# Kernel optimization log

Hardware: AMD Instinct MI355X
Metric: run time of the kernel (lower is better)

## Reference

```python
import jax, jax.numpy as jnp
import numpy as np

FEATURES = 1024
HEAD_DIM = 64
NUM_HEADS = 16
EPS = 1e-5


def setup_inputs() -> dict:
    key = jax.random.key(0)
    ks = jax.random.split(key, 6)
    x = jax.random.normal(ks[0], (2, 2048, FEATURES), dtype=jnp.float32)
    s_in = 1.0 / np.sqrt(FEATURES)
    s_hd = 1.0 / np.sqrt(NUM_HEADS * HEAD_DIM)
    return {
        "x": x,
        "gamma": jnp.ones((FEATURES,), jnp.float32),
        "beta": jnp.zeros((FEATURES,), jnp.float32),
        "Wq": jax.random.normal(ks[1], (FEATURES, NUM_HEADS * HEAD_DIM), jnp.float32) * s_in,
        "Wkv": jax.random.normal(ks[2], (FEATURES, 2 * HEAD_DIM), jnp.float32) * s_in,
        "Wo": jax.random.normal(ks[3], (NUM_HEADS * HEAD_DIM, FEATURES), jnp.float32) * s_hd,
        "bo": jax.random.normal(ks[4], (FEATURES,), jnp.float32) * s_hd,
    }


def reference(x, gamma, beta, Wq, Wkv, Wo, bo):
    # LayerNorm over last dim
    mu = jnp.mean(x, axis=-1, keepdims=True)
    var = jnp.mean(jnp.square(x - mu), axis=-1, keepdims=True)
    xn = (x - mu) * jax.lax.rsqrt(var + EPS) * gamma + beta

    b, t, _ = x.shape
    q = (xn @ Wq).reshape(b, t, NUM_HEADS, HEAD_DIM).transpose(0, 2, 1, 3)  # b h t d
    kv = xn @ Wkv  # b s 2d
    k, v = kv[..., :HEAD_DIM], kv[..., HEAD_DIM:]  # b s d (single shared head)

    scale = HEAD_DIM ** (-0.5)
    attn = jnp.einsum('bhtd,bsd->bhts', q, k) * scale
    attn = jax.nn.softmax(attn, axis=-1)
    out = jnp.einsum('bhts,bsd->bhtd', attn, v)
    out = out.transpose(0, 2, 1, 3).reshape(b, t, NUM_HEADS * HEAD_DIM)
    return out @ Wo + bo + x
```

## Files before the change

### kernel.cpp

```cpp
#include <hip/hip_runtime.h>

typedef __attribute__((ext_vector_type(8))) __bf16 bf16x8;
typedef __attribute__((ext_vector_type(4))) float floatx4;
typedef unsigned short u16;
typedef unsigned int u32;

#define KSCALE 0.18033688011112042f

__device__ __forceinline__ u16 f2bf(float f) {
    union { float f; u32 u; } v; v.f = f;
    u32 r = v.u + 0x7fffu + ((v.u >> 16) & 1u);
    return (u16)(r >> 16);
}

__device__ __forceinline__ u32 pk2bf(float a, float b) {
    union { float f; u32 u; } x, y; x.f = a; y.f = b;
    return __builtin_amdgcn_perm(y.u + 0x8000u, x.u + 0x8000u, 0x07060302);
}

__device__ __forceinline__ void gl_lds16(const u16* g, u16* l) {
    __builtin_amdgcn_global_load_lds((const __attribute__((address_space(1))) void*)g,
                                     (__attribute__((address_space(3))) void*)l, 16, 0, 0);
}

__global__ __launch_bounds__(256) void prep(const float* __restrict__ Wq, const float* __restrict__ Wkv,
                                            const float* __restrict__ Wo, const float* __restrict__ x,
                                            const float* __restrict__ gamma, const float* __restrict__ beta,
                                            u16* __restrict__ WqkvT, u16* __restrict__ WoT,
                                            u16* __restrict__ xn) {
    __shared__ float tile[64][68];
    __shared__ float ps[4], ps2[4];
    const int bx = blockIdx.x;
    const int t = threadIdx.x;
    if (bx < 768) {
        const int z = bx >> 8, rem = bx & 255;
        const int tr = (rem >> 4) * 64, tc = (rem & 15) * 64;
        const float* in = (z == 0) ? Wq : (z == 1 ? Wkv : Wo);
        u16* out = (z == 0) ? WqkvT : (z == 1 ? WqkvT + (size_t)1024 * 1024 : WoT);
        const int cols = (z == 1) ? 128 : 1024;
        if (tc >= cols) return;
        for (int p = 0; p < 4; p++) {
            int ri = (t >> 4) + p * 16;
            int ci = (t & 15) * 4;
            float4 v = *(const float4*)&in[(size_t)(tr + ri) * cols + tc + ci];
            tile[ri][ci + 0] = v.x; tile[ri][ci + 1] = v.y;
            tile[ri][ci + 2] = v.z; tile[ri][ci + 3] = v.w;
        }
        __syncthreads();
        for (int p = 0; p < 4; p++) {
            int oc = (t >> 4) + p * 16;
            int ir = (t & 15) * 4;
            float s = (z == 1 && (tc + oc) < 64) ? KSCALE : 1.0f;
            ushort4 o;
            o.x = f2bf(tile[ir + 0][oc] * s);
            o.y = f2bf(tile[ir + 1][oc] * s);
            o.z = f2bf(tile[ir + 2][oc] * s);
            o.w = f2bf(tile[ir + 3][oc] * s);
            *(ushort4*)&out[(size_t)(tc + oc) * 1024 + tr + ir] = o;
        }
    } else {
        const int row = bx - 768;
        const float* xr = x + (size_t)row * 1024;
        float4 v = *(const float4*)&xr[t * 4];
        float s = v.x + v.y + v.z + v.w;
        float s2 = v.x * v.x + v.y * v.y + v.z * v.z + v.w * v.w;
        for (int off = 1; off < 64; off <<= 1) {
            s += __shfl_xor(s, off, 64);
            s2 += __shfl_xor(s2, off, 64);
        }
        int w = t >> 6, lane = t & 63;
        if (lane == 0) { ps[w] = s; ps2[w] = s2; }
        __syncthreads();
        float S = ps[0] + ps[1] + ps[2] + ps[3];
        float S2 = ps2[0] + ps2[1] + ps2[2] + ps2[3];
        float mu = S * (1.0f / 1024.0f);
        float var = S2 * (1.0f / 1024.0f) - mu * mu;
        float rstd = rsqrtf(var + 1e-5f);
        ushort4 o;
        o.x = f2bf((v.x - mu) * rstd * gamma[t * 4 + 0] + beta[t * 4 + 0]);
        o.y = f2bf((v.y - mu) * rstd * gamma[t * 4 + 1] + beta[t * 4 + 1]);
        o.z = f2bf((v.z - mu) * rstd * gamma[t * 4 + 2] + beta[t * 4 + 2]);
        o.w = f2bf((v.w - mu) * rstd * gamma[t * 4 + 3] + beta[t * 4 + 3]);
        *(ushort4*)&xn[(size_t)row * 1024 + t * 4] = o;
    }
}

template <bool FINAL>
__global__ __launch_bounds__(256) void gemm_bt(const u16* __restrict__ A, const u16* __restrict__ BT,
                                               u16* __restrict__ Cb, float* __restrict__ Cf,
                                               const float* __restrict__ bias, const float* __restrict__ resid,
                                               u16* __restrict__ vt2, int M, int N, int K) {
    __shared__ u16 as_[128 * 32];
    __shared__ u16 bs_[128 * 32];
    const int t = threadIdx.x;
    const int w = t >> 6, lane = t & 63, q = lane >> 4, c = lane & 15;
    const int tm = blockIdx.y * 128, tn = blockIdx.x * 128;
    const int wm = (w & 1) * 64, wn = (w >> 1) * 64;

    const int srow = lane >> 2, sch = (lane & 3) * 8;
    const u16* ag0 = A + (size_t)(tm + w * 16 + srow) * K + sch;
    const u16* ag1 = ag0 + (size_t)64 * K;
    const u16* bg0 = BT + (size_t)(tn + w * 16 + srow) * K + sch;
    const u16* bg1 = bg0 + (size_t)64 * K;
    u16* al0 = as_ + (w * 16) * 32;
    u16* al1 = as_ + (64 + w * 16) * 32;
    u16* bl0 = bs_ + (w * 16) * 32;
    u16* bl1 = bs_ + (64 + w * 16) * 32;

    floatx4 acc[4][4];
    for (int i = 0; i < 4; i++)
        for (int j = 0; j < 4; j++) acc[i][j] = (floatx4){0.f, 0.f, 0.f, 0.f};

    for (int k0 = 0; k0 < K; k0 += 32) {
        __syncthreads();
        gl_lds16(ag0 + k0, al0);
        gl_lds16(ag1 + k0, al1);
        gl_lds16(bg0 + k0, bl0);
        gl_lds16(bg1 + k0, bl1);
        __syncthreads();
        bf16x8 af[4], bf[4];
#pragma unroll
        for (int i = 0; i < 4; i++) af[i] = *(const bf16x8*)&as_[(wm + i * 16 + c) * 32 + q * 8];
#pragma unroll
        for (int j = 0; j < 4; j++) bf[j] = *(const bf16x8*)&bs_[(wn + j * 16 + c) * 32 + q * 8];
#pragma unroll
        for (int i = 0; i < 4; i++)
#pragma unroll
            for (int j = 0; j < 4; j++)
                acc[i][j] = __builtin_amdgcn_mfma_f32_16x16x32_bf16(af[i], bf[j], acc[i][j], 0, 0, 0);
    }
#pragma unroll
    for (int i = 0; i < 4; i++)
#pragma unroll
        for (int j = 0; j < 4; j++)
#pragma unroll
            for (int r = 0; r < 4; r++) {
                int row = tm + wm + i * 16 + q * 4 + r;
                int col = tn + wn + j * 16 + c;
                float v = acc[i][j][r];
                if (FINAL) {
                    Cf[(size_t)row * N + col] = v + bias[col] + resid[(size_t)row * N + col];
                } else if (col < 1088) {
                    Cb[(size_t)row * N + col] = f2bf(v);
                } else {
                    int d = col - 1088;
                    int bb = row >> 11, sl = row & 2047;
                    int Bk = sl >> 5, u = sl & 31;
                    int up = ((u >> 2) & 3) * 8 + ((u >> 4) << 2) + (u & 3);
                    vt2[((size_t)(bb * 64 + d)) * 2048 + Bk * 32 + up] = f2bf(v);
                }
            }
}

union Vf { bf16x8 v; u32 w[4]; };

__global__ __launch_bounds__(512, 4) void attn5(const u16* __restrict__ qkv, const u16* __restrict__ vt2,
                                                u16* __restrict__ out) {
    __shared__ u16 ksm[2][64 * 64];
    __shared__ u16 vsm[2][64 * 64];
    const int t = threadIdx.x;
    const int w = t >> 6, lane = t & 63;
    const int q = lane >> 4, c = lane & 15;
    const int qt = blockIdx.x, hg = blockIdx.y, b = blockIdx.z;
    const int h = hg * 8 + w;
    const size_t qrow0 = (size_t)b * 2048 + qt * 16;
    const u16* kbase = qkv + (size_t)b * 2048 * 1152 + 1024;
    const u16* vbase = vt2 + (size_t)b * 64 * 2048;

    const int srow = w * 8 + (lane >> 3);
    const int sch = lane & 7;
    const int swz = (sch ^ (srow & 7)) * 8;
    const u16* kg = kbase + (size_t)srow * 1152 + swz;
    const u16* vg = vbase + (size_t)srow * 2048 + swz;
    u16* kl[2] = {&ksm[0][(w * 8) * 64], &ksm[1][(w * 8) * 64]};
    u16* vl[2] = {&vsm[0][(w * 8) * 64], &vsm[1][(w * 8) * 64]};

    bf16x8 qf[2];
#pragma unroll
    for (int kk = 0; kk < 2; kk++)
        qf[kk] = *(const bf16x8*)&qkv[(qrow0 + c) * 1152 + h * 64 + kk * 32 + q * 8];

    floatx4 O[4], Lacc;
#pragma unroll
    for (int di = 0; di < 4; di++) O[di] = (floatx4){0.f, 0.f, 0.f, 0.f};
    Lacc = (floatx4){0.f, 0.f, 0.f, 0.f};
    Vf ones;
    ones.w[0] = ones.w[1] = ones.w[2] = ones.w[3] = 0x3F803F80u;

    gl_lds16(kg, kl[0]);
    gl_lds16(vg, vl[0]);
    __syncthreads();

    const int c7 = c & 7;
    for (int tt = 0; tt < 32; tt++) {
        const int cur = tt & 1, nxt = cur ^ 1;
        if (tt < 31) {
            gl_lds16(kg + (size_t)(tt + 1) * 64 * 1152, kl[nxt]);
            gl_lds16(vg + (tt + 1) * 64, vl[nxt]);
        }

        bf16x8 kf[4][2];
        Vf vf[4][2];
#pragma unroll
        for (int ni = 0; ni < 4; ni++)
#pragma unroll
            for (int kk = 0; kk < 2; kk++)
                kf[ni][kk] = *(const bf16x8*)&ksm[cur][(ni * 16 + c) * 64 + (((kk * 4 + q) ^ c7) * 8)];
#pragma unroll
        for (int di = 0; di < 4; di++)
#pragma unroll
            for (int kk = 0; kk < 2; kk++)
                vf[di][kk].v = *(const bf16x8*)&vsm[cur][(di * 16 + c) * 64 + (((kk * 4 + q) ^ c7) * 8)];

        floatx4 sacc[4];
#pragma unroll
        for (int ni = 0; ni < 4; ni++) {
            floatx4 z = (floatx4){0.f, 0.f, 0.f, 0.f};
            z = __builtin_amdgcn_mfma_f32_16x16x32_bf16(kf[ni][0], qf[0], z, 0, 0, 0);
            z = __builtin_amdgcn_mfma_f32_16x16x32_bf16(kf[ni][1], qf[1], z, 0, 0, 0);
            sacc[ni] = z;
        }

        u32 pk[4][2];
#pragma unroll
        for (int ni = 0; ni < 4; ni++) {
            float p0 = exp2f(sacc[ni][0]);
            float p1 = exp2f(sacc[ni][1]);
            float p2 = exp2f(sacc[ni][2]);
            float p3 = exp2f(sacc[ni][3]);
            pk[ni][0] = pk2bf(p0, p1);
            pk[ni][1] = pk2bf(p2, p3);
        }

#pragma unroll
        for (int kk = 0; kk < 2; kk++) {
            Vf pf;
            pf.w[0] = pk[2 * kk][0];
            pf.w[1] = pk[2 * kk][1];
            pf.w[2] = pk[2 * kk + 1][0];
            pf.w[3] = pk[2 * kk + 1][1];
#pragma unroll
            for (int di = 0; di < 4; di++)
                O[di] = __builtin_amdgcn_mfma_f32_16x16x32_bf16(vf[di][kk].v, pf.v, O[di], 0, 0, 0);
            Lacc = __builtin_amdgcn_mfma_f32_16x16x32_bf16(ones.v, pf.v, Lacc, 0, 0, 0);
        }

        __syncthreads();
    }

    float inv = 1.0f / Lacc[0];
#pragma unroll
    for (int di = 0; di < 4; di++) {
        ushort4 o;
        o.x = f2bf(O[di][0] * inv);
        o.y = f2bf(O[di][1] * inv);
        o.z = f2bf(O[di][2] * inv);
        o.w = f2bf(O[di][3] * inv);
        *(ushort4*)&out[(qrow0 + c) * 1024 + h * 64 + di * 16 + q * 4] = o;
    }
}

extern "C" void kernel_launch(void* const* d_in, const int* in_sizes, int n_in,
                              void* d_out, int out_size, void* d_ws, size_t ws_size,
                              hipStream_t stream) {
    const float* x = (const float*)d_in[0];
    const float* gamma = (const float*)d_in[1];
    const float* beta = (const float*)d_in[2];
    const float* Wq = (const float*)d_in[3];
    const float* Wkv = (const float*)d_in[4];
    const float* Wo = (const float*)d_in[5];
    const float* bo = (const float*)d_in[6];
    float* out = (float*)d_out;

    u16* WqkvT = (u16*)d_ws;
    u16* WoT = WqkvT + (size_t)1152 * 1024;
    u16* xn = WoT + (size_t)1024 * 1024;
    u16* qkv = xn + (size_t)4096 * 1024;
    u16* vt2 = qkv + (size_t)4096 * 1152;
    u16* attnO = xn;

    prep<<<4864, 256, 0, stream>>>(Wq, Wkv, Wo, x, gamma, beta, WqkvT, WoT, xn);
    gemm_bt<false><<<dim3(9, 32), 256, 0, stream>>>(xn, WqkvT, qkv, nullptr, nullptr, nullptr, vt2,
                                                    4096, 1152, 1024);
    attn5<<<dim3(128, 2, 2), 512, 0, stream>>>(qkv, vt2, attnO);
    gemm_bt<true><<<dim3(8, 32), 256, 0, stream>>>(attnO, WoT, nullptr, out, bo, x, nullptr,
                                                   4096, 1024, 1024);
}
```

Before: 199.9 us.

## Shrink GEMM M-tile to 64 and double attention KV chunk per barrier

The GEMM tile drops from 128x128 to 64x128 rows, which doubles the grid (288→576 and 256→512 blocks) so the machine's many CUs are better filled, at the cost of less operand reuse per block. The attention kernel now stages 128 keys and values per double-buffered step and processes them in two 64-key sub-steps, halving the number of barriers and load rounds. This doubles the attention LDS use to 64KB per block, which may reduce how many blocks fit per CU.

After: 187.5 us. -6.2%, faster.

```diff
diff --git a/kernel.cpp b/kernel.cpp
--- a/kernel.cpp
+++ b/kernel.cpp
@@ -90,47 +90,44 @@
                                                u16* __restrict__ Cb, float* __restrict__ Cf,
                                                const float* __restrict__ bias, const float* __restrict__ resid,
                                                u16* __restrict__ vt2, int M, int N, int K) {
-    __shared__ u16 as_[128 * 32];
+    __shared__ u16 as_[64 * 32];
     __shared__ u16 bs_[128 * 32];
     const int t = threadIdx.x;
     const int w = t >> 6, lane = t & 63, q = lane >> 4, c = lane & 15;
-    const int tm = blockIdx.y * 128, tn = blockIdx.x * 128;
-    const int wm = (w & 1) * 64, wn = (w >> 1) * 64;
+    const int tm = blockIdx.y * 64, tn = blockIdx.x * 128;
+    const int wm = (w & 1) * 32, wn = (w >> 1) * 64;
 
     const int srow = lane >> 2, sch = (lane & 3) * 8;
-    const u16* ag0 = A + (size_t)(tm + w * 16 + srow) * K + sch;
-    const u16* ag1 = ag0 + (size_t)64 * K;
+    const u16* ag = A + (size_t)(tm + w * 16 + srow) * K + sch;
     const u16* bg0 = BT + (size_t)(tn + w * 16 + srow) * K + sch;
     const u16* bg1 = bg0 + (size_t)64 * K;
-    u16* al0 = as_ + (w * 16) * 32;
-    u16* al1 = as_ + (64 + w * 16) * 32;
+    u16* al = as_ + (w * 16) * 32;
     u16* bl0 = bs_ + (w * 16) * 32;
     u16* bl1 = bs_ + (64 + w * 16) * 32;
 
-    floatx4 acc[4][4];
-    for (int i = 0; i < 4; i++)
+    floatx4 acc[2][4];
+    for (int i = 0; i < 2; i++)
         for (int j = 0; j < 4; j++) acc[i][j] = (floatx4){0.f, 0.f, 0.f, 0.f};
 
     for (int k0 = 0; k0 < K; k0 += 32) {
         __syncthreads();
-        gl_lds16(ag0 + k0, al0);
-        gl_lds16(ag1 + k0, al1);
+        gl_lds16(ag + k0, al);
         gl_lds16(bg0 + k0, bl0);
         gl_lds16(bg1 + k0, bl1);
         __syncthreads();
-        bf16x8 af[4], bf[4];
-#pragma unroll
-        for (int i = 0; i < 4; i++) af[i] = *(const bf16x8*)&as_[(wm + i * 16 + c) * 32 + q * 8];
+        bf16x8 af[2], bf[4];
+#pragma unroll
+        for (int i = 0; i < 2; i++) af[i] = *(const bf16x8*)&as_[(wm + i * 16 + c) * 32 + q * 8];
 #pragma unroll
         for (int j = 0; j < 4; j++) bf[j] = *(const bf16x8*)&bs_[(wn + j * 16 + c) * 32 + q * 8];
 #pragma unroll
-        for (int i = 0; i < 4; i++)
+        for (int i = 0; i < 2; i++)
 #pragma unroll
             for (int j = 0; j < 4; j++)
                 acc[i][j] = __builtin_amdgcn_mfma_f32_16x16x32_bf16(af[i], bf[j], acc[i][j], 0, 0, 0);
     }
 #pragma unroll
-    for (int i = 0; i < 4; i++)
+    for (int i = 0; i < 2; i++)
 #pragma unroll
         for (int j = 0; j < 4; j++)
 #pragma unroll
@@ -154,10 +151,10 @@
 
 union Vf { bf16x8 v; u32 w[4]; };
 
-__global__ __launch_bounds__(512, 4) void attn5(const u16* __restrict__ qkv, const u16* __restrict__ vt2,
+__global__ __launch_bounds__(512, 4) void attn6(const u16* __restrict__ qkv, const u16* __restrict__ vt2,
                                                 u16* __restrict__ out) {
-    __shared__ u16 ksm[2][64 * 64];
-    __shared__ u16 vsm[2][64 * 64];
+    __shared__ u16 ksm[2][128 * 64];
+    __shared__ u16 vsm[2][2 * 64 * 64];
     const int t = threadIdx.x;
     const int w = t >> 6, lane = t & 63;
     const int q = lane >> 4, c = lane & 15;
@@ -167,13 +164,15 @@
     const u16* kbase = qkv + (size_t)b * 2048 * 1152 + 1024;
     const u16* vbase = vt2 + (size_t)b * 64 * 2048;
 
-    const int srow = w * 8 + (lane >> 3);
-    const int sch = lane & 7;
-    const int swz = (sch ^ (srow & 7)) * 8;
-    const u16* kg = kbase + (size_t)srow * 1152 + swz;
-    const u16* vg = vbase + (size_t)srow * 2048 + swz;
-    u16* kl[2] = {&ksm[0][(w * 8) * 64], &ksm[1][(w * 8) * 64]};
-    u16* vl[2] = {&vsm[0][(w * 8) * 64], &vsm[1][(w * 8) * 64]};
+    const int l3 = lane >> 3;
+    const int swz = ((lane & 7) ^ l3) * 8;
+    const u16* kg0 = kbase + (size_t)(w * 16 + l3) * 1152 + swz;
+    const u16* kg1 = kg0 + (size_t)8 * 1152;
+    const u16* vg = vbase + (size_t)(w * 8 + l3) * 2048 + swz;
+    u16* kl0[2] = {&ksm[0][(w * 16) * 64], &ksm[1][(w * 16) * 64]};
+    u16* kl1[2] = {&ksm[0][(w * 16 + 8) * 64], &ksm[1][(w * 16 + 8) * 64]};
+    u16* vl0[2] = {&vsm[0][(w * 8) * 64], &vsm[1][(w * 8) * 64]};
+    u16* vl1[2] = {&vsm[0][64 * 64 + (w * 8) * 64], &vsm[1][64 * 64 + (w * 8) * 64]};
 
     bf16x8 qf[2];
 #pragma unroll
@@ -187,62 +186,71 @@
     Vf ones;
     ones.w[0] = ones.w[1] = ones.w[2] = ones.w[3] = 0x3F803F80u;
 
-    gl_lds16(kg, kl[0]);
-    gl_lds16(vg, vl[0]);
+    gl_lds16(kg0, kl0[0]);
+    gl_lds16(kg1, kl1[0]);
+    gl_lds16(vg, vl0[0]);
+    gl_lds16(vg + 64, vl1[0]);
     __syncthreads();
 
     const int c7 = c & 7;
-    for (int tt = 0; tt < 32; tt++) {
-        const int cur = tt & 1, nxt = cur ^ 1;
-        if (tt < 31) {
-            gl_lds16(kg + (size_t)(tt + 1) * 64 * 1152, kl[nxt]);
-            gl_lds16(vg + (tt + 1) * 64, vl[nxt]);
-        }
-
-        bf16x8 kf[4][2];
-        Vf vf[4][2];
-#pragma unroll
-        for (int ni = 0; ni < 4; ni++)
-#pragma unroll
-            for (int kk = 0; kk < 2; kk++)
-                kf[ni][kk] = *(const bf16x8*)&ksm[cur][(ni * 16 + c) * 64 + (((kk * 4 + q) ^ c7) * 8)];
-#pragma unroll
-        for (int di = 0; di < 4; di++)
-#pragma unroll
-            for (int kk = 0; kk < 2; kk++)
-                vf[di][kk].v = *(const bf16x8*)&vsm[cur][(di * 16 + c) * 64 + (((kk * 4 + q) ^ c7) * 8)];
-
-        floatx4 sacc[4];
-#pragma unroll
-        for (int ni = 0; ni < 4; ni++) {
-            floatx4 z = (floatx4){0.f, 0.f, 0.f, 0.f};
-            z = __builtin_amdgcn_mfma_f32_16x16x32_bf16(kf[ni][0], qf[0], z, 0, 0, 0);
-            z = __builtin_amdgcn_mfma_f32_16x16x32_bf16(kf[ni][1], qf[1], z, 0, 0, 0);
-            sacc[ni] = z;
-        }
-
-        u32 pk[4][2];
-#pragma unroll
-        for (int ni = 0; ni < 4; ni++) {
-            float p0 = exp2f(sacc[ni][0]);
-            float p1 = exp2f(sacc[ni][1]);
-            float p2 = exp2f(sacc[ni][2]);
-            float p3 = exp2f(sacc[ni][3]);
-            pk[ni][0] = pk2bf(p0, p1);
-            pk[ni][1] = pk2bf(p2, p3);
-        }
-
-#pragma unroll
-        for (int kk = 0; kk < 2; kk++) {
-            Vf pf;
-            pf.w[0] = pk[2 * kk][0];
-            pf.w[1] = pk[2 * kk][1];
-            pf.w[2] = pk[2 * kk + 1][0];
-            pf.w[3] = pk[2 * kk + 1][1];
+    for (int g = 0; g < 16; g++) {
+        const int cur = g & 1, nxt = cur ^ 1;
+        if (g < 15) {
+            const size_t ko = (size_t)(g + 1) * 128 * 1152;
+            const int vo = (g + 1) * 128;
+            gl_lds16(kg0 + ko, kl0[nxt]);
+            gl_lds16(kg1 + ko, kl1[nxt]);
+            gl_lds16(vg + vo, vl0[nxt]);
+            gl_lds16(vg + vo + 64, vl1[nxt]);
+        }
+
+#pragma unroll
+        for (int st = 0; st < 2; st++) {
+            bf16x8 kf[4][2];
+            Vf vf[4][2];
+#pragma unroll
+            for (int ni = 0; ni < 4; ni++)
+#pragma unroll
+                for (int kk = 0; kk < 2; kk++)
+                    kf[ni][kk] = *(const bf16x8*)&ksm[cur][(st * 64 + ni * 16 + c) * 64 + (((kk * 4 + q) ^ c7) * 8)];
 #pragma unroll
             for (int di = 0; di < 4; di++)
-                O[di] = __builtin_amdgcn_mfma_f32_16x16x32_bf16(vf[di][kk].v, pf.v, O[di], 0, 0, 0);
-            Lacc = __builtin_amdgcn_mfma_f32_16x16x32_bf16(ones.v, pf.v, Lacc, 0, 0, 0);
+#pragma unroll
+                for (int kk = 0; kk < 2; kk++)
+                    vf[di][kk].v = *(const bf16x8*)&vsm[cur][st * 64 * 64 + (di * 16 + c) * 64 + (((kk * 4 + q) ^ c7) * 8)];
+
+            floatx4 sacc[4];
+#pragma unroll
+            for (int ni = 0; ni < 4; ni++) {
+                floatx4 z = (floatx4){0.f, 0.f, 0.f, 0.f};
+                z = __builtin_amdgcn_mfma_f32_16x16x32_bf16(kf[ni][0], qf[0], z, 0, 0, 0);
+                z = __builtin_amdgcn_mfma_f32_16x16x32_bf16(kf[ni][1], qf[1], z, 0, 0, 0);
+                sacc[ni] = z;
+            }
+
+            u32 pk[4][2];
+#pragma unroll
+            for (int ni = 0; ni < 4; ni++) {
+                float p0 = exp2f(sacc[ni][0]);
+                float p1 = exp2f(sacc[ni][1]);
+                float p2 = exp2f(sacc[ni][2]);
+                float p3 = exp2f(sacc[ni][3]);
+                pk[ni][0] = pk2bf(p0, p1);
+                pk[ni][1] = pk2bf(p2, p3);
+            }
+
+#pragma unroll
+            for (int kk = 0; kk < 2; kk++) {
+                Vf pf;
+                pf.w[0] = pk[2 * kk][0];
+                pf.w[1] = pk[2 * kk][1];
+                pf.w[2] = pk[2 * kk + 1][0];
+                pf.w[3] = pk[2 * kk + 1][1];
+#pragma unroll
+                for (int di = 0; di < 4; di++)
+                    O[di] = __builtin_amdgcn_mfma_f32_16x16x32_bf16(vf[di][kk].v, pf.v, O[di], 0, 0, 0);
+                Lacc = __builtin_amdgcn_mfma_f32_16x16x32_bf16(ones.v, pf.v, Lacc, 0, 0, 0);
+            }
         }
 
         __syncthreads();
@@ -280,9 +288,9 @@
     u16* attnO = xn;
 
     prep<<<4864, 256, 0, stream>>>(Wq, Wkv, Wo, x, gamma, beta, WqkvT, WoT, xn);
-    gemm_bt<false><<<dim3(9, 32), 256, 0, stream>>>(xn, WqkvT, qkv, nullptr, nullptr, nullptr, vt2,
+    gemm_bt<false><<<dim3(9, 64), 256, 0, stream>>>(xn, WqkvT, qkv, nullptr, nullptr, nullptr, vt2,
                                                     4096, 1152, 1024);
-    attn5<<<dim3(128, 2, 2), 512, 0, stream>>>(qkv, vt2, attnO);
-    gemm_bt<true><<<dim3(8, 32), 256, 0, stream>>>(attnO, WoT, nullptr, out, bo, x, nullptr,
+    attn6<<<dim3(128, 2, 2), 512, 0, stream>>>(qkv, vt2, attnO);
+    gemm_bt<true><<<dim3(8, 64), 256, 0, stream>>>(attnO, WoT, nullptr, out, bo, x, nullptr,
                                                    4096, 1024, 1024);
 }
```
